# Kernel optimization log

Hardware: AMD Instinct MI355X
Metric: run time of the kernel (lower is better)

The kernel has to match this reference:

```python
import jax, jax.numpy as jnp
import numpy as np

B, S, D = 2, 2048, 2048
H, DH, DR = 16, 128, 64
DC_KV, DC_Q = 512, 1536
ROPE_BASE = 10000.0


def _rope(t):
    """Apply rotate-half RoPE over the last dim of t: [B, S, H, DR]."""
    s, dr = t.shape[1], t.shape[-1]
    inv_freq = 1.0 / (ROPE_BASE ** (jnp.arange(0, dr, 2, dtype=jnp.float32) / dr))
    ang = jnp.arange(s, dtype=jnp.float32)[:, None] * inv_freq  # [S, DR/2]
    cos = jnp.tile(jnp.cos(ang), (1, 2))[None, :, None, :]  # [1,S,1,DR]
    sin = jnp.tile(jnp.sin(ang), (1, 2))[None, :, None, :]
    t1, t2 = jnp.split(t, 2, axis=-1)
    rot = jnp.concatenate([-t2, t1], axis=-1)
    return t * cos + rot * sin


def setup_inputs() -> dict:
    key = jax.random.key(0)
    ks = jax.random.split(key, 18)
    g = lambda k, shp: (jax.random.normal(k, shp, dtype=jnp.float32) * 0.02)
    return {
        "x": jax.random.normal(ks[0], (B, S, D), dtype=jnp.float32),
        "Wkd": g(ks[1], (DC_KV, D)),   "bkd": jnp.zeros((DC_KV,), jnp.float32),
        "Wqd": g(ks[2], (DC_Q, D)),    "bqd": jnp.zeros((DC_Q,), jnp.float32),
        "Wku": g(ks[3], (H * DH, DC_KV)), "bku": jnp.zeros((H * DH,), jnp.float32),
        "Wvu": g(ks[4], (H * DH, DC_KV)), "bvu": jnp.zeros((H * DH,), jnp.float32),
        "Wqu": g(ks[5], (H * DH, DC_Q)),  "bqu": jnp.zeros((H * DH,), jnp.float32),
        "Wkr": g(ks[6], (H * DR, D)),     "bkr": jnp.zeros((H * DR,), jnp.float32),
        "Wqr": g(ks[7], (H * DR, DC_Q)),  "bqr": jnp.zeros((H * DR,), jnp.float32),
        "Wo": g(ks[8], (D, H * DH)),      "bo": jnp.zeros((D,), jnp.float32),
    }


def reference(x, Wkd, bkd, Wqd, bqd, Wku, bku, Wvu, bvu, Wqu, bqu,
              Wkr, bkr, Wqr, bqr, Wo, bo):
    b, s, _ = x.shape
    # 1. Compress to latent spaces
    kv_c = x @ Wkd.T + bkd          # [B,S,DC_KV]
    q_c = x @ Wqd.T + bqd           # [B,S,DC_Q]
    # 2-3. Up-project content / value / rope features
    k_cnt = (kv_c @ Wku.T + bku).reshape(b, s, H, DH)
    v = (kv_c @ Wvu.T + bvu).reshape(b, s, H, DH)
    q_cnt = (q_c @ Wqu.T + bqu).reshape(b, s, H, DH)
    k_r = (x @ Wkr.T + bkr).reshape(b, s, H, DR)      # keys rope from input (eq. 3)
    q_r = (q_c @ Wqr.T + bqr).reshape(b, s, H, DR)    # query rope from latent (eq. 8)
    # 5. Partial RoPE: rotate position features, concat with content
    q_full = jnp.concatenate([q_cnt, _rope(q_r)], axis=-1)  # [B,S,H,DH+DR]
    k_full = jnp.concatenate([k_cnt, _rope(k_r)], axis=-1)
    # 7. Manual causal attention (mscale = 1)
    scale = 1.0 / jnp.sqrt(jnp.float32(DH + DR))
    scores = jnp.einsum("bqhd,bkhd->bhqk", q_full, k_full) * scale
    causal = jnp.tril(jnp.ones((s, s), dtype=bool))
    scores = jnp.where(causal[None, None], scores, jnp.float32(-1e9))
    probs = jax.nn.softmax(scores, axis=-1)
    attn = jnp.einsum("bhqk,bkhd->bqhd", probs, v).reshape(b, s, H * DH)
    # 9. Output projection
    return attn @ Wo.T + bo
```

## Files before the change

kernel.cpp:

```cpp
#include <hip/hip_runtime.h>
#include <stdint.h>
#include <stddef.h>

#define BB 2
#define SS 2048
#define DD 2048
#define HH 16
#define DHH 128
#define DRR 64
#define DCKV 512
#define DCQ 1536

typedef __attribute__((ext_vector_type(8))) short short8;
typedef __attribute__((ext_vector_type(4))) short short4v;
typedef __attribute__((ext_vector_type(4))) float f32x4;
typedef unsigned int u32;

__device__ __forceinline__ short f2bf(float x) {
  unsigned u = __float_as_uint(x);
  u += 0x7fffu + ((u >> 16) & 1u);
  return (short)(u >> 16);
}
__device__ __forceinline__ float bf2f(short s) {
  return __uint_as_float(((unsigned)(unsigned short)s) << 16);
}

#define BAR_NOVM() asm volatile("s_waitcnt lgkmcnt(0)\n\ts_barrier" ::: "memory")

__device__ __forceinline__ void gl2lds16(const short* g, short* l) {
  __builtin_amdgcn_global_load_lds(
      (const __attribute__((address_space(1))) u32*)g,
      (__attribute__((address_space(3))) u32*)l, 16, 0, 0);
}

__global__ __launch_bounds__(256) void cast_all_kernel(
    const float* __restrict__ x,   const float* __restrict__ Wkd,
    const float* __restrict__ Wqd, const float* __restrict__ Wkr,
    const float* __restrict__ Wqu, const float* __restrict__ Wqr,
    const float* __restrict__ Wku, const float* __restrict__ Wvu,
    const float* __restrict__ Wo,
    short* __restrict__ xb, short* __restrict__ w1, short* __restrict__ w2,
    short* __restrict__ w3, short* __restrict__ wob) {
  int i = blockIdx.x * 256 + threadIdx.x;
  const float* s; short* d; int j;
  if (i < 2097152)      { s = x;   d = xb;                        j = i; }
  else if (i < 2359296) { s = Wkd; d = w1;                        j = i - 2097152; }
  else if (i < 3145728) { s = Wqd; d = w1 + (size_t)512 * 2048;   j = i - 2359296; }
  else if (i < 3670016) { s = Wkr; d = w1 + (size_t)2048 * 2048;  j = i - 3145728; }
  else if (i < 4456448) { s = Wqu; d = w2;                        j = i - 3670016; }
  else if (i < 4849664) { s = Wqr; d = w2 + (size_t)2048 * 1536;  j = i - 4456448; }
  else if (i < 5111808) { s = Wku; d = w3;                        j = i - 4849664; }
  else if (i < 5373952) { s = Wvu; d = w3 + (size_t)2048 * 512;   j = i - 5111808; }
  else                  { s = Wo;  d = wob;                       j = i - 5373952; }
  f32x4 f = ((const f32x4*)s)[j];
  short4v o;
  o[0] = f2bf(f[0]); o[1] = f2bf(f[1]); o[2] = f2bf(f[2]); o[3] = f2bf(f[3]);
  ((short4v*)d)[j] = o;
}

__global__ __launch_bounds__(256) void concat_bias_kernel(
    const float* bkd, const float* bqd, const float* bkr,
    const float* bqu, const float* bqr, const float* bku, const float* bvu,
    float* cb1, float* cb2, float* cb3) {
  int idx = blockIdx.x * 256 + threadIdx.x;
  if (idx < 3072) {
    cb1[idx] = idx < 512 ? bkd[idx] : (idx < 2048 ? bqd[idx - 512] : bkr[idx - 2048]);
  } else if (idx < 6144) {
    int j = idx - 3072;
    cb2[j] = j < 2048 ? bqu[j] : bqr[j - 2048];
  } else if (idx < 10240) {
    int j = idx - 6144;
    cb3[j] = j < 2048 ? bku[j] : bvu[j - 2048];
  }
}

template<int MODE>
__global__ __launch_bounds__(256) void gemm_bt(const short* __restrict__ A, int lda,
                                               const short* __restrict__ Bm, int ldb,
                                               const float* __restrict__ bias,
                                               void* __restrict__ Cout, void* __restrict__ out2,
                                               int M, int N, int K) {
  __shared__ __align__(16) short sA[128 * 32];
  __shared__ __align__(16) short sB[128 * 32];
  const int tid = threadIdx.x;
  const int w = tid >> 6, L = tid & 63, quad = L >> 4, lc = L & 15;
  const int wm = w >> 1, wn = w & 1;
  const int tm = blockIdx.x * 128, tn = blockIdx.y * 128;
  const int lrow = L >> 2, lch = (L & 3) * 8;
  f32x4 acc[4][4] = {};
  const int nk = K >> 5;
  for (int kt = 0; kt < nk; ++kt) {
    const int k0 = kt << 5;
    __syncthreads();
    {
      int sub = w * 2;
      gl2lds16(A + (size_t)(tm + sub * 16 + lrow) * lda + k0 + lch, &sA[sub * 512]);
      gl2lds16(A + (size_t)(tm + sub * 16 + 16 + lrow) * lda + k0 + lch, &sA[sub * 512 + 512]);
      gl2lds16(Bm + (size_t)(tn + sub * 16 + lrow) * ldb + k0 + lch, &sB[sub * 512]);
      gl2lds16(Bm + (size_t)(tn + sub * 16 + 16 + lrow) * ldb + k0 + lch, &sB[sub * 512 + 512]);
    }
    __syncthreads();
    short8 af[4], bfr[4];
#pragma unroll
    for (int ms = 0; ms < 4; ++ms)
      af[ms] = *(const short8*)&sA[(wm * 64 + ms * 16 + lc) * 32 + quad * 8];
#pragma unroll
    for (int ns = 0; ns < 4; ++ns)
      bfr[ns] = *(const short8*)&sB[(wn * 64 + ns * 16 + lc) * 32 + quad * 8];
#pragma unroll
    for (int ms = 0; ms < 4; ++ms)
#pragma unroll
      for (int ns = 0; ns < 4; ++ns)
        acc[ms][ns] = __builtin_amdgcn_mfma_f32_16x16x32_bf16(af[ms], bfr[ns], acc[ms][ns], 0, 0, 0);
  }
#pragma unroll
  for (int ms = 0; ms < 4; ++ms) {
    int row = tm + wm * 64 + ms * 16 + quad * 4;
#pragma unroll
    for (int ns = 0; ns < 4; ++ns) {
      int col = tn + wn * 64 + ns * 16 + lc;
      float bv = bias[col];
      if (MODE == 3 && col >= 2048) {
        int j = col - 2048, h_ = j >> 7, dh = j & 127;
        int b_ = row >> 11, s0 = row & 2047;
        short4v pk;
#pragma unroll
        for (int r = 0; r < 4; ++r) pk[r] = f2bf(acc[ms][ns][r] + bv);
        *(short4v*)((short*)out2 + (((size_t)(b_ * HH + h_)) * DHH + dh) * SS + s0) = pk;
      } else {
#pragma unroll
        for (int r = 0; r < 4; ++r) {
          float vv = acc[ms][ns][r] + bv;
          int rrow = row + r;
          if (MODE == 0)      ((short*)Cout)[(size_t)rrow * N + col] = f2bf(vv);
          else if (MODE == 1) ((float*)Cout)[(size_t)rrow * N + col] = vv;
          else {
            if (col < 2048) {
              int b_ = rrow >> 11, s_ = rrow & 2047, h_ = col >> 7, d_ = col & 127;
              ((short*)Cout)[(((size_t)(b_ * HH + h_)) * SS + s_) * 192 + d_] = f2bf(vv);
            } else {
              ((short*)out2)[(size_t)rrow * 1024 + (col - 2048)] = f2bf(vv);
            }
          }
        }
      }
    }
  }
}

__global__ __launch_bounds__(256) void rope_kernel(const short* __restrict__ rin,
                                                   int rstride, int roff,
                                                   short* __restrict__ full) {
  int idx = blockIdx.x * 256 + threadIdx.x;
  int i = idx & 31, h = (idx >> 5) & 15, s = (idx >> 9) & 2047, b = idx >> 20;
  const short* base = rin + ((size_t)(b * SS + s)) * rstride + roff + h * DRR;
  float t1 = bf2f(base[i]), t2 = bf2f(base[i + 32]);
  float invf = expf(-9.210340371976184f * (float)i * (1.0f / 32.0f));
  float ang = (float)s * invf;
  float c = cosf(ang), sn = sinf(ang);
  short* ob = full + (((size_t)(b * HH + h)) * SS + s) * 192 + 128;
  ob[i]      = f2bf(t1 * c - t2 * sn);
  ob[i + 32] = f2bf(t1 * sn + t2 * c);
}

__device__ __forceinline__ float quad_max(float v) {
  v = fmaxf(v, __shfl_xor(v, 1));
  v = fmaxf(v, __shfl_xor(v, 2));
  v = fmaxf(v, __shfl_xor(v, 4));
  v = fmaxf(v, __shfl_xor(v, 8));
  return v;
}
__device__ __forceinline__ float quad_sum(float v) {
  v += __shfl_xor(v, 1); v += __shfl_xor(v, 2);
  v += __shfl_xor(v, 4); v += __shfl_xor(v, 8);
  return v;
}

__global__ __launch_bounds__(256, 2) void mla_flash_kernel(const short* __restrict__ Qf,
                                                           const short* __restrict__ Kf,
                                                           const short* __restrict__ Vt,
                                                           float* __restrict__ Opart,
                                                           float* __restrict__ Mpart,
                                                           float* __restrict__ Lpart,
                                                           short* __restrict__ attn) {
  const int bid = blockIdx.x;
  const int g0 = (bid & 7) * 160 + (bid >> 3);
  const int bh = g0 / 40, xc = g0 - bh * 40;
  int qt, c;
  if (xc < 4)       { qt = xc;                  c = 0; }
  else if (xc < 12) { qt = 4 + ((xc - 4) >> 1);  c = (xc - 4) & 1; }
  else if (xc < 24) { qt = 8 + (xc - 12) / 3;    c = (xc - 12) % 3; }
  else              { qt = 12 + ((xc - 24) >> 2); c = (xc - 24) & 3; }
  const int nc = (qt + 4) >> 2;
  const int k8 = c * 8;
  const int klim = 2 * qt + 2;
  const int kend = (k8 + 8 < klim) ? k8 + 8 : klim;
  const int slot = bh * 40 + xc;

  const int h = bh & 15, b = bh >> 4;
  const int tid = threadIdx.x, w = tid >> 6, L = tid & 63, quad = L >> 4, lc = L & 15;
  __shared__ __align__(16) short sK[12288];
  __shared__ __align__(16) short sV[8192];
  short* Pf = sK;

  const short* Qb = Qf + ((size_t)bh) * SS * 192;
  const short* Kb = Kf + ((size_t)bh) * SS * 192;
  const short* Vb = Vt + ((size_t)bh) * DHH * SS;

  const int qrow0 = qt * 128 + w * 32;
  short8 qa[2][6];
#pragma unroll
  for (int ms = 0; ms < 2; ++ms)
#pragma unroll
    for (int kk = 0; kk < 6; ++kk)
      qa[ms][kk] = *(const short8*)(Qb + (size_t)(qrow0 + ms * 16 + lc) * 192 + kk * 32 + quad * 8);

  f32x4 O[2][8] = {};
  float mrow[2][4], lrow[2][4];
#pragma unroll
  for (int ms = 0; ms < 2; ++ms)
#pragma unroll
    for (int r = 0; r < 4; ++r) { mrow[ms][r] = -1e30f; lrow[ms][r] = 0.f; }

  const int srow_ = tid >> 2, sq_ = tid & 3;
  const int sslot = srow_ * 4 + (sq_ ^ ((srow_ >> 1) & 3));
  const int vrow_ = tid >> 3, vch_ = tid & 7;
  short8 g[6], gv[4];
#pragma unroll
  for (int i = 0; i < 6; ++i)
    g[i] = *(const short8*)(Kb + (size_t)(k8 * 64 + srow_) * 192 + i * 32 + sq_ * 8);
#pragma unroll
  for (int j = 0; j < 4; ++j)
    gv[j] = *(const short8*)(Vb + (size_t)(j * 32 + vrow_) * SS + k8 * 64 + vch_ * 8);

  for (int kt = k8; kt < kend; ++kt) {
    BAR_NOVM();
#pragma unroll
    for (int i = 0; i < 6; ++i)
      *(short8*)&sK[(i * 256 + sslot) * 8] = g[i];
#pragma unroll
    for (int j = 0; j < 4; ++j) {
      int row = j * 32 + vrow_;
      *(short8*)&sV[row * 64 + ((vch_ ^ (row & 7)) << 3)] = gv[j];
    }
    if (kt + 1 < kend) {
#pragma unroll
      for (int i = 0; i < 6; ++i)
        g[i] = *(const short8*)(Kb + (size_t)((kt + 1) * 64 + srow_) * 192 + i * 32 + sq_ * 8);
#pragma unroll
      for (int j = 0; j < 4; ++j)
        gv[j] = *(const short8*)(Vb + (size_t)(j * 32 + vrow_) * SS + (kt + 1) * 64 + vch_ * 8);
    }
    BAR_NOVM();
    f32x4 sc[2][4] = {};
#pragma unroll
    for (int kk = 0; kk < 6; ++kk)
#pragma unroll
      for (int ns = 0; ns < 4; ++ns) {
        int rr = ns * 16 + lc;
        short8 kb = *(const short8*)&sK[(kk * 256 + rr * 4 + (quad ^ ((rr >> 1) & 3))) * 8];
        sc[0][ns] = __builtin_amdgcn_mfma_f32_16x16x32_bf16(qa[0][kk], kb, sc[0][ns], 0, 0, 0);
        sc[1][ns] = __builtin_amdgcn_mfma_f32_16x16x32_bf16(qa[1][kk], kb, sc[1][ns], 0, 0, 0);
      }
    const float scale = 0.07216878364870322f;
#pragma unroll
    for (int ms = 0; ms < 2; ++ms)
#pragma unroll
      for (int ns = 0; ns < 4; ++ns)
#pragma unroll
        for (int r = 0; r < 4; ++r) {
          float vv = sc[ms][ns][r] * scale;
          if (kt * 64 + ns * 16 + lc > qrow0 + ms * 16 + quad * 4 + r) vv = -1e30f;
          sc[ms][ns][r] = vv;
        }
#pragma unroll
    for (int ms = 0; ms < 2; ++ms)
#pragma unroll
      for (int r = 0; r < 4; ++r) {
        float mx = fmaxf(fmaxf(sc[ms][0][r], sc[ms][1][r]), fmaxf(sc[ms][2][r], sc[ms][3][r]));
        mx = quad_max(mx);
        float mnew = fmaxf(mrow[ms][r], mx);
        float alpha = __expf(mrow[ms][r] - mnew);
        mrow[ms][r] = mnew;
        float ps = 0.f;
#pragma unroll
        for (int ns = 0; ns < 4; ++ns) {
          float p = __expf(sc[ms][ns][r] - mnew);
          sc[ms][ns][r] = p;
          ps += p;
        }
        ps = quad_sum(ps);
        lrow[ms][r] = lrow[ms][r] * alpha + ps;
#pragma unroll
        for (int n = 0; n < 8; ++n) O[ms][n][r] *= alpha;
      }
    BAR_NOVM();
#pragma unroll
    for (int ms = 0; ms < 2; ++ms)
#pragma unroll
      for (int ns = 0; ns < 4; ++ns)
#pragma unroll
        for (int r = 0; r < 4; ++r) {
          int row = w * 32 + ms * 16 + quad * 4 + r;
          int col = ns * 16 + lc;
          Pf[row * 64 + (((col >> 3) ^ (row & 7)) << 3) + (col & 7)] = f2bf(sc[ms][ns][r]);
        }
#pragma unroll
    for (int kk2 = 0; kk2 < 2; ++kk2) {
      int r0 = w * 32 + lc, r1 = w * 32 + 16 + lc;
      short8 pa0 = *(const short8*)&Pf[r0 * 64 + (((kk2 * 4 + quad) ^ (r0 & 7)) << 3)];
      short8 pa1 = *(const short8*)&Pf[r1 * 64 + (((kk2 * 4 + quad) ^ (r1 & 7)) << 3)];
      short8 vb[8];
#pragma unroll
      for (int n = 0; n < 8; ++n) {
        int rr = n * 16 + lc;
        vb[n] = *(const short8*)&sV[rr * 64 + (((kk2 * 4 + quad) ^ (lc & 7)) << 3)];
      }
#pragma unroll
      for (int n = 0; n < 8; ++n) {
        O[0][n] = __builtin_amdgcn_mfma_f32_16x16x32_bf16(pa0, vb[n], O[0][n], 0, 0, 0);
        O[1][n] = __builtin_amdgcn_mfma_f32_16x16x32_bf16(pa1, vb[n], O[1][n], 0, 0, 0);
      }
    }
  }
  if (nc == 1) {
#pragma unroll
    for (int ms = 0; ms < 2; ++ms)
#pragma unroll
      for (int r = 0; r < 4; ++r) {
        float inv = 1.0f / lrow[ms][r];
        int srow = qt * 128 + w * 32 + ms * 16 + quad * 4 + r;
        short* dst = attn + ((size_t)b * SS + srow) * 2048 + h * 128;
#pragma unroll
        for (int n = 0; n < 8; ++n)
          dst[n * 16 + lc] = f2bf(O[ms][n][r] * inv);
      }
  } else {
    float* Ob = Opart + (size_t)slot * 16384;
#pragma unroll
    for (int ms = 0; ms < 2; ++ms)
#pragma unroll
      for (int r = 0; r < 4; ++r) {
        int row = w * 32 + ms * 16 + quad * 4 + r;
#pragma unroll
        for (int n = 0; n < 8; ++n)
          Ob[(size_t)row * 128 + n * 16 + lc] = O[ms][n][r];
      }
    if (lc == 0) {
#pragma unroll
      for (int ms = 0; ms < 2; ++ms)
#pragma unroll
        for (int r = 0; r < 4; ++r) {
          int row = w * 32 + ms * 16 + quad * 4 + r;
          Mpart[slot * 128 + row] = mrow[ms][r];
          Lpart[slot * 128 + row] = lrow[ms][r];
        }
    }
  }
}

__global__ __launch_bounds__(256) void combine_kernel(const float* __restrict__ Op,
                                                      const float* __restrict__ Mp,
                                                      const float* __restrict__ Lp,
                                                      short* __restrict__ attn) {
  int idx = blockIdx.x * 256 + threadIdx.x;
  int col = idx & 127;
  int r = (idx >> 7) & 127;
  int t = idx >> 14;
  int bh = t / 12, qt = (t - bh * 12) + 4;
  int nc = (qt + 4) >> 2;
  int cbase;
  if (qt < 8)       cbase = 4 + 2 * (qt - 4);
  else if (qt < 12) cbase = 12 + 3 * (qt - 8);
  else              cbase = 24 + 4 * (qt - 12);
  int slot0 = bh * 40 + cbase;
  float mc[4];
#pragma unroll
  for (int cc = 0; cc < 4; ++cc)
    mc[cc] = (cc < nc) ? Mp[(size_t)(slot0 + cc) * 128 + r] : -1e30f;
  float M = fmaxf(fmaxf(mc[0], mc[1]), fmaxf(mc[2], mc[3]));
  float den = 0.f, acc = 0.f;
#pragma unroll
  for (int cc = 0; cc < 4; ++cc) {
    if (cc < nc) {
      float e = __expf(mc[cc] - M);
      den += e * Lp[(size_t)(slot0 + cc) * 128 + r];
      acc += e * Op[(size_t)(slot0 + cc) * 16384 + (size_t)r * 128 + col];
    }
  }
  int b = bh >> 4, hh = bh & 15;
  int srow = qt * 128 + r;
  attn[((size_t)b * SS + srow) * 2048 + hh * 128 + col] = f2bf(acc / den);
}

extern "C" void kernel_launch(void* const* d_in, const int* in_sizes, int n_in,
                              void* d_out, int out_size, void* d_ws, size_t ws_size,
                              hipStream_t stream) {
  const float* x   = (const float*)d_in[0];
  const float* Wkd = (const float*)d_in[1];
  const float* bkd = (const float*)d_in[2];
  const float* Wqd = (const float*)d_in[3];
  const float* bqd = (const float*)d_in[4];
  const float* Wku = (const float*)d_in[5];
  const float* bku = (const float*)d_in[6];
  const float* Wvu = (const float*)d_in[7];
  const float* bvu = (const float*)d_in[8];
  const float* Wqu = (const float*)d_in[9];
  const float* bqu = (const float*)d_in[10];
  const float* Wkr = (const float*)d_in[11];
  const float* bkr = (const float*)d_in[12];
  const float* Wqr = (const float*)d_in[13];
  const float* bqr = (const float*)d_in[14];
  const float* Wo  = (const float*)d_in[15];
  const float* bo  = (const float*)d_in[16];

  char* ws = (char*)d_ws;
  size_t off = 0;
  auto alloc = [&](size_t elems, size_t esz) -> void* {
    void* p = (void*)(ws + off);
    off += elems * esz;
    off = (off + 255) & ~(size_t)255;
    return p;
  };
  const int MS = BB * SS;
  short* xb    = (short*)alloc((size_t)MS * DD, 2);
  short* cbuf  = (short*)alloc((size_t)MS * 3072, 2);
  short* qrbuf = (short*)alloc((size_t)MS * 1024, 2);
  short* vbuf  = (short*)alloc((size_t)MS * 2048, 2);
  short* w1    = (short*)alloc((size_t)3072 * 2048, 2);
  short* w2    = (short*)alloc((size_t)3072 * 1536, 2);
  short* w3    = (short*)alloc((size_t)4096 * 512, 2);
  short* wob   = (short*)alloc((size_t)2048 * 2048, 2);
  float* cb1   = (float*)alloc(3072, 4);
  float* cb2   = (float*)alloc(3072, 4);
  float* cb3   = (float*)alloc(4096, 4);
  short* qfull = (short*)alloc((size_t)BB * HH * SS * 192, 2);
  short* kfull = (short*)alloc((size_t)BB * HH * SS * 192, 2);
  short* vt    = (short*)alloc((size_t)BB * HH * DHH * SS, 2);
  short* attn  = (short*)alloc((size_t)MS * 2048, 2);
  if (off > ws_size) return;

  float* Opart = (float*)ws;
  float* Mpart = (float*)(ws + (size_t)1280 * 16384 * 4);
  float* Lpart = (float*)(ws + (size_t)1280 * 16384 * 4 + (size_t)1280 * 128 * 4);

  dim3 blk(256);
  cast_all_kernel<<<dim3(25088), blk, 0, stream>>>(x, Wkd, Wqd, Wkr, Wqu, Wqr, Wku, Wvu, Wo,
                                                   xb, w1, w2, w3, wob);
  concat_bias_kernel<<<dim3(40), blk, 0, stream>>>(bkd, bqd, bkr, bqu, bqr, bku, bvu,
                                                   cb1, cb2, cb3);

  gemm_bt<0><<<dim3(32, 24), blk, 0, stream>>>(xb, DD, w1, DD, cb1, cbuf, nullptr,
                                               MS, 3072, DD);
  gemm_bt<2><<<dim3(32, 24), blk, 0, stream>>>(cbuf + 512, 3072, w2, DCQ, cb2, qfull, qrbuf,
                                               MS, 3072, DCQ);
  gemm_bt<3><<<dim3(32, 32), blk, 0, stream>>>(cbuf, 3072, w3, DCKV, cb3, kfull, vt,
                                               MS, 4096, DCKV);

  rope_kernel<<<dim3(BB * SS * HH * 32 / 256), blk, 0, stream>>>(qrbuf, 1024, 0, qfull);
  rope_kernel<<<dim3(BB * SS * HH * 32 / 256), blk, 0, stream>>>(cbuf, 3072, 2048, kfull);

  mla_flash_kernel<<<dim3(1280), blk, 0, stream>>>(qfull, kfull, vt, Opart, Mpart, Lpart, attn);
  combine_kernel<<<dim3(24576), blk, 0, stream>>>(Opart, Mpart, Lpart, attn);

  gemm_bt<1><<<dim3(32, 16), blk, 0, stream>>>(attn, DD, wob, DD, bo, d_out, nullptr,
                                               MS, DD, DD);
}
```

Measured before the change: 607.9 us.

## Use 8 waves of 16 query rows each in MLA flash kernel

The flash attention block moves from 4 waves handling 32 query rows each to 8 waves handling 16 rows each, with the K/V tile loads split across 512 threads. P gets its own shared buffer instead of aliasing sK, which removes one barrier per K tile. The aim is more latency hiding and fewer registers per wave (launch bounds 512,4). In exchange, each K/V fragment read from shared memory now feeds half as many MFMAs, and shared memory per block grows.

```diff
diff --git a/kernel.cpp b/kernel.cpp
--- a/kernel.cpp
+++ b/kernel.cpp
@@ -176,7 +176,7 @@
   return v;
 }
 
-__global__ __launch_bounds__(256, 2) void mla_flash_kernel(const short* __restrict__ Qf,
+__global__ __launch_bounds__(512, 4) void mla_flash_kernel(const short* __restrict__ Qf,
                                                            const short* __restrict__ Kf,
                                                            const short* __restrict__ Vt,
                                                            float* __restrict__ Opart,
@@ -201,160 +201,134 @@
   const int tid = threadIdx.x, w = tid >> 6, L = tid & 63, quad = L >> 4, lc = L & 15;
   __shared__ __align__(16) short sK[12288];
   __shared__ __align__(16) short sV[8192];
-  short* Pf = sK;
+  __shared__ __align__(16) short Pf[8192];
 
   const short* Qb = Qf + ((size_t)bh) * SS * 192;
   const short* Kb = Kf + ((size_t)bh) * SS * 192;
   const short* Vb = Vt + ((size_t)bh) * DHH * SS;
 
-  const int qrow0 = qt * 128 + w * 32;
-  short8 qa[2][6];
-#pragma unroll
-  for (int ms = 0; ms < 2; ++ms)
-#pragma unroll
-    for (int kk = 0; kk < 6; ++kk)
-      qa[ms][kk] = *(const short8*)(Qb + (size_t)(qrow0 + ms * 16 + lc) * 192 + kk * 32 + quad * 8);
-
-  f32x4 O[2][8] = {};
-  float mrow[2][4], lrow[2][4];
-#pragma unroll
-  for (int ms = 0; ms < 2; ++ms)
-#pragma unroll
-    for (int r = 0; r < 4; ++r) { mrow[ms][r] = -1e30f; lrow[ms][r] = 0.f; }
-
-  const int srow_ = tid >> 2, sq_ = tid & 3;
-  const int sslot = srow_ * 4 + (sq_ ^ ((srow_ >> 1) & 3));
+  const int qrow0 = qt * 128 + w * 16;
+  short8 qa[6];
+#pragma unroll
+  for (int kk = 0; kk < 6; ++kk)
+    qa[kk] = *(const short8*)(Qb + (size_t)(qrow0 + lc) * 192 + kk * 32 + quad * 8);
+
+  f32x4 O[8] = {};
+  float mrow[4], lrow[4];
+#pragma unroll
+  for (int r = 0; r < 4; ++r) { mrow[r] = -1e30f; lrow[r] = 0.f; }
+
+  const int krow_ = (tid & 255) >> 2, kq_ = tid & 3, kseg0 = tid >> 8;
+  const int kslot = krow_ * 4 + (kq_ ^ ((krow_ >> 1) & 3));
   const int vrow_ = tid >> 3, vch_ = tid & 7;
-  short8 g[6], gv[4];
-#pragma unroll
-  for (int i = 0; i < 6; ++i)
-    g[i] = *(const short8*)(Kb + (size_t)(k8 * 64 + srow_) * 192 + i * 32 + sq_ * 8);
-#pragma unroll
-  for (int j = 0; j < 4; ++j)
-    gv[j] = *(const short8*)(Vb + (size_t)(j * 32 + vrow_) * SS + k8 * 64 + vch_ * 8);
+  short8 g[3], gv[2];
+#pragma unroll
+  for (int i = 0; i < 3; ++i)
+    g[i] = *(const short8*)(Kb + (size_t)(k8 * 64 + krow_) * 192 + (kseg0 + 2 * i) * 32 + kq_ * 8);
+#pragma unroll
+  for (int i = 0; i < 2; ++i)
+    gv[i] = *(const short8*)(Vb + (size_t)(vrow_ + i * 64) * SS + k8 * 64 + vch_ * 8);
 
   for (int kt = k8; kt < kend; ++kt) {
     BAR_NOVM();
 #pragma unroll
-    for (int i = 0; i < 6; ++i)
-      *(short8*)&sK[(i * 256 + sslot) * 8] = g[i];
-#pragma unroll
-    for (int j = 0; j < 4; ++j) {
-      int row = j * 32 + vrow_;
-      *(short8*)&sV[row * 64 + ((vch_ ^ (row & 7)) << 3)] = gv[j];
+    for (int i = 0; i < 3; ++i)
+      *(short8*)&sK[((kseg0 + 2 * i) * 256 + kslot) * 8] = g[i];
+#pragma unroll
+    for (int i = 0; i < 2; ++i) {
+      int row = vrow_ + i * 64;
+      *(short8*)&sV[row * 64 + ((vch_ ^ (row & 7)) << 3)] = gv[i];
     }
     if (kt + 1 < kend) {
 #pragma unroll
-      for (int i = 0; i < 6; ++i)
-        g[i] = *(const short8*)(Kb + (size_t)((kt + 1) * 64 + srow_) * 192 + i * 32 + sq_ * 8);
-#pragma unroll
-      for (int j = 0; j < 4; ++j)
-        gv[j] = *(const short8*)(Vb + (size_t)(j * 32 + vrow_) * SS + (kt + 1) * 64 + vch_ * 8);
+      for (int i = 0; i < 3; ++i)
+        g[i] = *(const short8*)(Kb + (size_t)((kt + 1) * 64 + krow_) * 192 + (kseg0 + 2 * i) * 32 + kq_ * 8);
+#pragma unroll
+      for (int i = 0; i < 2; ++i)
+        gv[i] = *(const short8*)(Vb + (size_t)(vrow_ + i * 64) * SS + (kt + 1) * 64 + vch_ * 8);
     }
     BAR_NOVM();
-    f32x4 sc[2][4] = {};
+    f32x4 sc[4] = {};
 #pragma unroll
     for (int kk = 0; kk < 6; ++kk)
 #pragma unroll
       for (int ns = 0; ns < 4; ++ns) {
         int rr = ns * 16 + lc;
         short8 kb = *(const short8*)&sK[(kk * 256 + rr * 4 + (quad ^ ((rr >> 1) & 3))) * 8];
-        sc[0][ns] = __builtin_amdgcn_mfma_f32_16x16x32_bf16(qa[0][kk], kb, sc[0][ns], 0, 0, 0);
-        sc[1][ns] = __builtin_amdgcn_mfma_f32_16x16x32_bf16(qa[1][kk], kb, sc[1][ns], 0, 0, 0);
+        sc[ns] = __builtin_amdgcn_mfma_f32_16x16x32_bf16(qa[kk], kb, sc[ns], 0, 0, 0);
       }
     const float scale = 0.07216878364870322f;
 #pragma unroll
-    for (int ms = 0; ms < 2; ++ms)
-#pragma unroll
-      for (int ns = 0; ns < 4; ++ns)
-#pragma unroll
-        for (int r = 0; r < 4; ++r) {
-          float vv = sc[ms][ns][r] * scale;
-          if (kt * 64 + ns * 16 + lc > qrow0 + ms * 16 + quad * 4 + r) vv = -1e30f;
-          sc[ms][ns][r] = vv;
-        }
-#pragma unroll
-    for (int ms = 0; ms < 2; ++ms)
+    for (int ns = 0; ns < 4; ++ns)
 #pragma unroll
       for (int r = 0; r < 4; ++r) {
-        float mx = fmaxf(fmaxf(sc[ms][0][r], sc[ms][1][r]), fmaxf(sc[ms][2][r], sc[ms][3][r]));
-        mx = quad_max(mx);
-        float mnew = fmaxf(mrow[ms][r], mx);
-        float alpha = __expf(mrow[ms][r] - mnew);
-        mrow[ms][r] = mnew;
-        float ps = 0.f;
-#pragma unroll
-        for (int ns = 0; ns < 4; ++ns) {
-          float p = __expf(sc[ms][ns][r] - mnew);
-          sc[ms][ns][r] = p;
-          ps += p;
-        }
-        ps = quad_sum(ps);
-        lrow[ms][r] = lrow[ms][r] * alpha + ps;
-#pragma unroll
-        for (int n = 0; n < 8; ++n) O[ms][n][r] *= alpha;
-      }
-    BAR_NOVM();
-#pragma unroll
-    for (int ms = 0; ms < 2; ++ms)
-#pragma unroll
-      for (int ns = 0; ns < 4; ++ns)
-#pragma unroll
-        for (int r = 0; r < 4; ++r) {
-          int row = w * 32 + ms * 16 + quad * 4 + r;
-          int col = ns * 16 + lc;
-          Pf[row * 64 + (((col >> 3) ^ (row & 7)) << 3) + (col & 7)] = f2bf(sc[ms][ns][r]);
-        }
+        float vv = sc[ns][r] * scale;
+        if (kt * 64 + ns * 16 + lc > qrow0 + quad * 4 + r) vv = -1e30f;
+        sc[ns][r] = vv;
+      }
+#pragma unroll
+    for (int r = 0; r < 4; ++r) {
+      float mx = fmaxf(fmaxf(sc[0][r], sc[1][r]), fmaxf(sc[2][r], sc[3][r]));
+      mx = quad_max(mx);
+      float mnew = fmaxf(mrow[r], mx);
+      float alpha = __expf(mrow[r] - mnew);
+      mrow[r] = mnew;
+      float ps = 0.f;
+#pragma unroll
+      for (int ns = 0; ns < 4; ++ns) {
+        float p = __expf(sc[ns][r] - mnew);
+        sc[ns][r] = p;
+        ps += p;
+      }
+      ps = quad_sum(ps);
+      lrow[r] = lrow[r] * alpha + ps;
+#pragma unroll
+      for (int n = 0; n < 8; ++n) O[n][r] *= alpha;
+    }
+#pragma unroll
+    for (int ns = 0; ns < 4; ++ns)
+#pragma unroll
+      for (int r = 0; r < 4; ++r) {
+        int row = w * 16 + quad * 4 + r;
+        int col = ns * 16 + lc;
+        Pf[row * 64 + (((col >> 3) ^ (row & 7)) << 3) + (col & 7)] = f2bf(sc[ns][r]);
+      }
 #pragma unroll
     for (int kk2 = 0; kk2 < 2; ++kk2) {
-      int r0 = w * 32 + lc, r1 = w * 32 + 16 + lc;
-      short8 pa0 = *(const short8*)&Pf[r0 * 64 + (((kk2 * 4 + quad) ^ (r0 & 7)) << 3)];
-      short8 pa1 = *(const short8*)&Pf[r1 * 64 + (((kk2 * 4 + quad) ^ (r1 & 7)) << 3)];
-      short8 vb[8];
+      short8 pa = *(const short8*)&Pf[(w * 16 + lc) * 64 + (((kk2 * 4 + quad) ^ (lc & 7)) << 3)];
 #pragma unroll
       for (int n = 0; n < 8; ++n) {
-        int rr = n * 16 + lc;
-        vb[n] = *(const short8*)&sV[rr * 64 + (((kk2 * 4 + quad) ^ (lc & 7)) << 3)];
-      }
-#pragma unroll
-      for (int n = 0; n < 8; ++n) {
-        O[0][n] = __builtin_amdgcn_mfma_f32_16x16x32_bf16(pa0, vb[n], O[0][n], 0, 0, 0);
-        O[1][n] = __builtin_amdgcn_mfma_f32_16x16x32_bf16(pa1, vb[n], O[1][n], 0, 0, 0);
+        short8 vb = *(const short8*)&sV[(n * 16 + lc) * 64 + (((kk2 * 4 + quad) ^ (lc & 7)) << 3)];
+        O[n] = __builtin_amdgcn_mfma_f32_16x16x32_bf16(pa, vb, O[n], 0, 0, 0);
       }
     }
   }
   if (nc == 1) {
 #pragma unroll
-    for (int ms = 0; ms < 2; ++ms)
-#pragma unroll
-      for (int r = 0; r < 4; ++r) {
-        float inv = 1.0f / lrow[ms][r];
-        int srow = qt * 128 + w * 32 + ms * 16 + quad * 4 + r;
-        short* dst = attn + ((size_t)b * SS + srow) * 2048 + h * 128;
-#pragma unroll
-        for (int n = 0; n < 8; ++n)
-          dst[n * 16 + lc] = f2bf(O[ms][n][r] * inv);
-      }
+    for (int r = 0; r < 4; ++r) {
+      float inv = 1.0f / lrow[r];
+      int srow = qrow0 + quad * 4 + r;
+      short* dst = attn + ((size_t)b * SS + srow) * 2048 + h * 128;
+#pragma unroll
+      for (int n = 0; n < 8; ++n)
+        dst[n * 16 + lc] = f2bf(O[n][r] * inv);
+    }
   } else {
     float* Ob = Opart + (size_t)slot * 16384;
 #pragma unroll
-    for (int ms = 0; ms < 2; ++ms)
+    for (int r = 0; r < 4; ++r) {
+      int row = w * 16 + quad * 4 + r;
+#pragma unroll
+      for (int n = 0; n < 8; ++n)
+        Ob[(size_t)row * 128 + n * 16 + lc] = O[n][r];
+    }
+    if (lc == 0) {
 #pragma unroll
       for (int r = 0; r < 4; ++r) {
-        int row = w * 32 + ms * 16 + quad * 4 + r;
-#pragma unroll
-        for (int n = 0; n < 8; ++n)
-          Ob[(size_t)row * 128 + n * 16 + lc] = O[ms][n][r];
-      }
-    if (lc == 0) {
-#pragma unroll
-      for (int ms = 0; ms < 2; ++ms)
-#pragma unroll
-        for (int r = 0; r < 4; ++r) {
-          int row = w * 32 + ms * 16 + quad * 4 + r;
-          Mpart[slot * 128 + row] = mrow[ms][r];
-          Lpart[slot * 128 + row] = lrow[ms][r];
-        }
+        int row = w * 16 + quad * 4 + r;
+        Mpart[slot * 128 + row] = mrow[r];
+        Lpart[slot * 128 + row] = lrow[r];
+      }
     }
   }
 }
@@ -460,7 +434,7 @@
   rope_kernel<<<dim3(BB * SS * HH * 32 / 256), blk, 0, stream>>>(qrbuf, 1024, 0, qfull);
   rope_kernel<<<dim3(BB * SS * HH * 32 / 256), blk, 0, stream>>>(cbuf, 3072, 2048, kfull);
 
-  mla_flash_kernel<<<dim3(1280), blk, 0, stream>>>(qfull, kfull, vt, Opart, Mpart, Lpart, attn);
+  mla_flash_kernel<<<dim3(1280), dim3(512), 0, stream>>>(qfull, kfull, vt, Opart, Mpart, Lpart, attn);
   combine_kernel<<<dim3(24576), blk, 0, stream>>>(Opart, Mpart, Lpart, attn);
 
   gemm_bt<1><<<dim3(32, 16), blk, 0, stream>>>(attn, DD, wob, DD, bo, d_out, nullptr,
```

Measured after the change: 598.8 us. Within noise of the previous version (-1.5%).
